# Optimization experiments

Hardware: AMD Instinct MI355X
Metric: run time of the kernel (lower is better)

The kernel has to match this reference:

```python
import jax, jax.numpy as jnp
import numpy as np

B, S, H, NH = 2, 2048, 4096, 32
D = H // NH  # head_dim = 128
ROPE_THETA = 10000.0


def setup_inputs() -> dict:
    key = jax.random.key(0)
    k0, k1, k2 = jax.random.split(key, 3)
    hidden_states = jax.random.normal(k0, (B, S, H), dtype=jnp.float32) * 0.02
    w_pack = jax.random.normal(k1, (H, 3 * H), dtype=jnp.float32) * 0.02  # fused QKV weight
    w_o = jax.random.normal(k2, (H, H), dtype=jnp.float32) * 0.02         # o_proj weight
    positions = jnp.broadcast_to(jnp.arange(S, dtype=jnp.int32), (B, S))
    return {"positions": positions, "hidden_states": hidden_states, "w_pack": w_pack, "w_o": w_o}


def _rope(x, positions):
    # neox-style rotary embedding (vLLM get_rope default), x: [B, S, NH, D]
    half = D // 2
    inv_freq = 1.0 / (ROPE_THETA ** (jnp.arange(0, half, dtype=jnp.float32) * 2.0 / D))
    freqs = positions.astype(jnp.float32)[..., None] * inv_freq  # [B, S, half]
    cos = jnp.cos(freqs)[:, :, None, :]  # [B, S, 1, half]
    sin = jnp.sin(freqs)[:, :, None, :]
    x1, x2 = x[..., :half], x[..., half:]
    return jnp.concatenate([x1 * cos - x2 * sin, x2 * cos + x1 * sin], axis=-1)


def reference(positions, hidden_states, w_pack, w_o):
    # fused QKV projection
    qkv = jnp.einsum('bsh,hf->bsf', hidden_states, w_pack)
    q, k, v = jnp.split(qkv, 3, axis=-1)
    q = q.reshape(B, S, NH, D)
    k = k.reshape(B, S, NH, D)
    v = v.reshape(B, S, NH, D)
    # RoPE on q, k
    q = _rope(q, positions)
    k = _rope(k, positions)
    # causal scaled dot-product attention
    scale = D ** -0.5
    scores = jnp.einsum('bqhd,bkhd->bhqk', q, k) * scale  # [B, NH, S, S]
    causal = jnp.tril(jnp.ones((S, S), dtype=bool))
    scores = jnp.where(causal[None, None], scores, jnp.finfo(scores.dtype).min)
    probs = jax.nn.softmax(scores, axis=-1)
    out = jnp.einsum('bhqk,bkhd->bqhd', probs, v).reshape(B, S, H)
    # output projection
    return jnp.einsum('bsh,hf->bsf', out, w_o)
```

## Files before the change

kernel.cpp:

```cpp
#include <hip/hip_runtime.h>

#define Sdim   2048
#define Hdim   4096
#define NHEADS 32
#define Dh     128
#define Mrows  4096
#define QKVLD  12288

typedef __attribute__((ext_vector_type(8))) short short8;
typedef __attribute__((ext_vector_type(4))) short short4v;
typedef __attribute__((ext_vector_type(4))) float f32x4;
typedef __attribute__((ext_vector_type(4))) float float4v;

__device__ __forceinline__ short f2bf(float f) {
  union { float f; unsigned u; } x; x.f = f;
  unsigned r = x.u + 0x7fffu + ((x.u >> 16) & 1u);
  return (short)(r >> 16);
}
__device__ __forceinline__ float bf2f(short s) {
  union { unsigned u; float f; } x; x.u = ((unsigned)(unsigned short)s) << 16;
  return x.f;
}

__device__ __forceinline__ void gload_lds16(const void* g, void* l) {
  __builtin_amdgcn_global_load_lds(
      (const __attribute__((address_space(1))) void*)g,
      (__attribute__((address_space(3))) void*)l, 16, 0, 0);
}

__global__ void k_prep(const float* __restrict__ hidden, short* __restrict__ Hbf,
                       const float* __restrict__ w_pack, short* __restrict__ Wpt) {
  __shared__ float t[64][65];
  const int tid = threadIdx.x;
  if (blockIdx.x < 8192) {
    int idx = blockIdx.x * 256 + tid;
    const float4v* s = (const float4v*)hidden + (size_t)idx * 2;
    float4v a = s[0], b = s[1];
    short8 o;
    o[0] = f2bf(a.x); o[1] = f2bf(a.y); o[2] = f2bf(a.z); o[3] = f2bf(a.w);
    o[4] = f2bf(b.x); o[5] = f2bf(b.y); o[6] = f2bf(b.z); o[7] = f2bf(b.w);
    *((short8*)Hbf + idx) = o;
  } else {
    const int idx = blockIdx.x - 8192;
    const int c0 = (idx % 192) * 64, r0 = (idx / 192) * 64;
    const int ir = tid >> 4, ic = (tid & 15) << 2;
#pragma unroll
    for (int p = 0; p < 4; ++p) {
      const float4v v = *(const float4v*)(w_pack + (size_t)(r0 + p * 16 + ir) * 12288 + c0 + ic);
      t[p * 16 + ir][ic] = v.x; t[p * 16 + ir][ic + 1] = v.y;
      t[p * 16 + ir][ic + 2] = v.z; t[p * 16 + ir][ic + 3] = v.w;
    }
    __syncthreads();
    const int oc = tid >> 3, orr = (tid & 7) << 3;
#pragma unroll
    for (int p = 0; p < 2; ++p) {
      int c = p * 32 + oc;
      short8 o;
#pragma unroll
      for (int j = 0; j < 8; ++j) o[j] = f2bf(t[orr + j][c]);
      *(short8*)(Wpt + (size_t)(c0 + c) * 4096 + r0 + orr) = o;
    }
  }
}

__device__ __forceinline__ void stage_half256(const short* G, int ld, int row0, int kcol,
                                              char* lds, int tid) {
#pragma unroll
  for (int j = 0; j < 2; ++j) {
    int p = j * 512 + tid;
    int r = p >> 3;
    int c = ((p & 7) ^ (r & 7)) << 3;
    gload_lds16(G + (size_t)(row0 + r) * ld + kcol + c,
                lds + ((j * 512 + (tid & 448)) << 4));
  }
}

#define MFMA_Q(qm, qn)                                                                   \
  do {                                                                                   \
    __builtin_amdgcn_s_setprio(1);                                                       \
    _Pragma("unroll")                                                                    \
    for (int m4 = 0; m4 < 4; ++m4)                                                       \
      _Pragma("unroll")                                                                  \
      for (int n2 = 0; n2 < 2; ++n2) {                                                   \
        acc[(qm)*4+m4][(qn)*2+n2] = __builtin_amdgcn_mfma_f32_16x16x32_bf16(             \
            av[m4][0], bv[(qn)*2+n2][0], acc[(qm)*4+m4][(qn)*2+n2], 0, 0, 0);            \
        acc[(qm)*4+m4][(qn)*2+n2] = __builtin_amdgcn_mfma_f32_16x16x32_bf16(             \
            av[m4][1], bv[(qn)*2+n2][1], acc[(qm)*4+m4][(qn)*2+n2], 0, 0, 0);            \
      }                                                                                  \
    __builtin_amdgcn_s_setprio(0);                                                       \
  } while (0)

#define PH_BARRIER()                    \
  do {                                  \
    __builtin_amdgcn_s_barrier();       \
    __builtin_amdgcn_sched_barrier(0);  \
  } while (0)

template<int MODE>
__global__ __launch_bounds__(512, 2) void k_gemm256(const short* __restrict__ A, int lda,
                                                    const short* __restrict__ Bt, int ldb,
                                                    void* __restrict__ Cp, int ldc,
                                                    int Ndim, int Kdim,
                                                    const int* __restrict__ positions,
                                                    short* __restrict__ Vtg) {
  __shared__ __align__(16) char smem[131072];
  const int tid  = threadIdx.x;
  const int lane = tid & 63;
  const int wave = tid >> 6;
  const int lo = lane & 15, hi = lane >> 4;
  const int wr = wave >> 2, wc = wave & 3;

  const int nblk = gridDim.x;
  const int lid = (blockIdx.x & 7) * (nblk >> 3) + (blockIdx.x >> 3);
  const int nbn = Ndim >> 8;
  const int bm0 = (lid / nbn) << 8;
  const int bn0 = (lid % nbn) << 8;

  f32x4 acc[8][4];
#pragma unroll
  for (int i = 0; i < 8; ++i)
#pragma unroll
    for (int j = 0; j < 4; ++j) acc[i][j] = (f32x4){0.f, 0.f, 0.f, 0.f};

  short8 av[4][2], bv[4][2];
  const int swz = (lo & 7) << 4;

  stage_half256(Bt, ldb, bn0,       0, smem + 32768,         tid);
  stage_half256(Bt, ldb, bn0 + 128, 0, smem + 32768 + 16384, tid);
  stage_half256(A,  lda, bm0,       0, smem,                 tid);
  stage_half256(A,  lda, bm0 + 128, 0, smem + 16384,         tid);

  const int NK = Kdim >> 6;
  for (int kt = 0; kt < NK; ++kt) {
    const int cur = kt & 1;
    const char* Ab = smem + cur * 65536 + wr * 16384;
    const char* Bb = smem + cur * 65536 + 32768;
    char* nA = smem + (cur ^ 1) * 65536;
    char* nB = nA + 32768;
    const int kc = (kt + 1) << 6;
    const bool pf = (kt + 1 < NK);

    if (pf) {
      stage_half256(Bt, ldb, bn0,       kc, nB,         tid);
      stage_half256(Bt, ldb, bn0 + 128, kc, nB + 16384, tid);
      asm volatile("s_waitcnt vmcnt(4)" ::: "memory");
    } else {
      asm volatile("s_waitcnt vmcnt(0)" ::: "memory");
    }
    PH_BARRIER();
#pragma unroll
    for (int m4 = 0; m4 < 4; ++m4)
#pragma unroll
      for (int ks = 0; ks < 2; ++ks)
        av[m4][ks] = *(const short8*)(Ab + (m4 * 16 + lo) * 128 + ((ks * 64 + hi * 16) ^ swz));
#pragma unroll
    for (int ni = 0; ni < 2; ++ni)
#pragma unroll
      for (int ks = 0; ks < 2; ++ks)
        bv[ni][ks] = *(const short8*)(Bb + (wc * 16 + ni * 64 + lo) * 128 + ((ks * 64 + hi * 16) ^ swz));
    MFMA_Q(0, 0);
#pragma unroll
    for (int ni = 2; ni < 4; ++ni)
#pragma unroll
      for (int ks = 0; ks < 2; ++ks)
        bv[ni][ks] = *(const short8*)(Bb + (wc * 16 + ni * 64 + lo) * 128 + ((ks * 64 + hi * 16) ^ swz));

    if (pf) {
      stage_half256(A, lda, bm0,       kc, nA,         tid);
      stage_half256(A, lda, bm0 + 128, kc, nA + 16384, tid);
    }
    PH_BARRIER();
    MFMA_Q(0, 1);
#pragma unroll
    for (int m4 = 0; m4 < 4; ++m4)
#pragma unroll
      for (int ks = 0; ks < 2; ++ks)
        av[m4][ks] = *(const short8*)(Ab + ((64 + m4 * 16 + lo) * 128) + ((ks * 64 + hi * 16) ^ swz));

    PH_BARRIER();
    MFMA_Q(1, 0);

    PH_BARRIER();
    MFMA_Q(1, 1);
  }

  if (MODE == 0) {
#pragma unroll
    for (int mi = 0; mi < 8; ++mi)
#pragma unroll
      for (int r = 0; r < 4; ++r) {
        int row = bm0 + wr * 128 + mi * 16 + hi * 4 + r;
#pragma unroll
        for (int ni = 0; ni < 4; ++ni) {
          int col = bn0 + wc * 16 + ni * 64 + lo;
          ((float*)Cp)[(size_t)row * ldc + col] = acc[mi][ni][r];
        }
      }
  } else if (bn0 < 8192) {
    short* qkvb = (short*)Cp;
    const int dd = wc * 16 + lo;
    const float inv = exp2f((float)dd * -0.2076205059304570f);
    const int row00 = bm0 + wr * 128 + hi * 4;
    float cm, sm, c1, s1, c16, s16;
    sincosf((float)positions[row00] * inv, &sm, &cm);
    sincosf(inv, &s1, &c1);
    sincosf(16.0f * inv, &s16, &c16);
#pragma unroll
    for (int mi = 0; mi < 8; ++mi) {
      float c = cm, s = sm;
#pragma unroll
      for (int r = 0; r < 4; ++r) {
        int row = row00 + mi * 16 + r;
        size_t base = (size_t)row * ldc + bn0 + wc * 16 + lo;
        float x1 = acc[mi][0][r], x2 = acc[mi][1][r];
        qkvb[base]       = f2bf(x1 * c - x2 * s);
        qkvb[base + 64]  = f2bf(x2 * c + x1 * s);
        float x3 = acc[mi][2][r], x4 = acc[mi][3][r];
        qkvb[base + 128] = f2bf(x3 * c - x4 * s);
        qkvb[base + 192] = f2bf(x4 * c + x3 * s);
        float cn = c * c1 - s * s1, sn = s * c1 + c * s1;
        c = cn; s = sn;
      }
      float cn = cm * c16 - sm * s16, sn = sm * c16 + cm * s16;
      cm = cn; sm = sn;
    }
  } else {
    const int b = bm0 >> 11;
    const int s0 = (bm0 & 2047) + wr * 128;
#pragma unroll
    for (int mi = 0; mi < 8; ++mi)
#pragma unroll
      for (int ni = 0; ni < 4; ++ni) {
        int col = bn0 - 8192 + wc * 16 + ni * 64 + lo;
        int h = col >> 7, d = col & 127;
        short4v o;
#pragma unroll
        for (int r = 0; r < 4; ++r) o[r] = f2bf(acc[mi][ni][r]);
        *(short4v*)(Vtg + (size_t)((b * 32 + h) * 128 + d) * Sdim + s0 + mi * 16 + hi * 4) = o;
      }
  }
}

__device__ __forceinline__ void stage_kv(const short* Kb, const short* Vtb, int kv0,
                                         char* kbuf, char* vbuf, int tid, int wave) {
#pragma unroll
  for (int i = 0; i < 4; ++i) {
    int p = i * 256 + tid;
    int r = p >> 4;
    int c = (p & 15) ^ (r & 7);
    gload_lds16(Kb + (size_t)(kv0 + r) * QKVLD + (c << 3),
                kbuf + ((i * 256 + wave * 64) << 4));
  }
#pragma unroll
  for (int i = 0; i < 4; ++i) {
    int p = i * 256 + tid;
    int r = p >> 3;
    int c = (p & 7) ^ (r & 7);
    gload_lds16(Vtb + (size_t)r * Sdim + kv0 + (c << 3),
                vbuf + ((i * 256 + wave * 64) << 4));
  }
}

__global__ __launch_bounds__(256, 2) void k_attn(short* __restrict__ qkv,
                                                 const short* __restrict__ Vt,
                                                 const float* __restrict__ w_o,
                                                 short* __restrict__ Wot) {
  __shared__ __align__(16) char smem[81920];
  const int tid  = threadIdx.x;

  if (blockIdx.x >= 1024) {
    float (*t)[65] = (float(*)[65])smem;
    const int idx = blockIdx.x - 1024;
    const int c0 = (idx & 63) << 6, r0 = (idx >> 6) << 6;
    const int ir = tid >> 4, ic = (tid & 15) << 2;
#pragma unroll
    for (int p = 0; p < 4; ++p) {
      const float4v v = *(const float4v*)(w_o + (size_t)(r0 + p * 16 + ir) * 4096 + c0 + ic);
      t[p * 16 + ir][ic] = v.x; t[p * 16 + ir][ic + 1] = v.y;
      t[p * 16 + ir][ic + 2] = v.z; t[p * 16 + ir][ic + 3] = v.w;
    }
    __syncthreads();
    const int oc = tid >> 3, orr = (tid & 7) << 3;
#pragma unroll
    for (int p = 0; p < 2; ++p) {
      int c = p * 32 + oc;
      short8 o;
#pragma unroll
      for (int j = 0; j < 8; ++j) o[j] = f2bf(t[orr + j][c]);
      *(short8*)(Wot + (size_t)(c0 + c) * 4096 + r0 + orr) = o;
    }
    return;
  }

  const int lane = tid & 63;
  const int wave = tid >> 6;
  const int lo = lane & 15, hi = lane >> 4;

  const int bid = blockIdx.x;
  const int lid = (bid & 7) * 128 + (bid >> 3);
  const int bh = lid >> 4;
  const int qt = 15 - (lid & 15);
  const int b = bh >> 5, h = bh & 31;
  const int q0 = qt << 7;

  short* base = qkv + (size_t)b * Sdim * QKVLD;
  const short* Qb = base + h * Dh;
  const short* Kb = base + Hdim + h * Dh;
  const short* Vtb = Vt + (size_t)(b * 32 + h) * 128 * Sdim;
  const int qrow0 = q0 + wave * 32;

  short* Pw = (short*)(smem + 65536 + wave * 4096);

  const float SEXP = 0.088388347648318447f * 1.4426950408889634f;

  short8 qf[2][4];
#pragma unroll
  for (int mi = 0; mi < 2; ++mi)
#pragma unroll
    for (int ks = 0; ks < 4; ++ks) {
      qf[mi][ks] = *(const short8*)(Qb + (size_t)(qrow0 + mi * 16 + lo) * QKVLD + ks * 32 + hi * 8);
#pragma unroll
      for (int j = 0; j < 8; ++j)
        qf[mi][ks][j] = f2bf(bf2f(qf[mi][ks][j]) * SEXP);
    }

  f32x4 acc_o[2][9];
  float m_run[2][4];
#pragma unroll
  for (int mi = 0; mi < 2; ++mi) {
#pragma unroll
    for (int nf = 0; nf < 9; ++nf) acc_o[mi][nf] = (f32x4){0.f, 0.f, 0.f, 0.f};
#pragma unroll
    for (int r = 0; r < 4; ++r) m_run[mi][r] = -1e30f;
  }

  short8 vones;
#pragma unroll
  for (int j = 0; j < 8; ++j) vones[j] = (short)0x3F80;

  const int nkv = (q0 + 128) >> 6;
  const int swz = (lo & 7) << 4;

  stage_kv(Kb, Vtb, 0, smem, smem + 16384, tid, wave);
  __syncthreads();

  int cur = 0;
  for (int kvt = 0; kvt < nkv; ++kvt) {
    const int kv0 = kvt << 6;
    if (kvt + 1 < nkv)
      stage_kv(Kb, Vtb, kv0 + 64, smem + (cur ^ 1) * 32768,
               smem + (cur ^ 1) * 32768 + 16384, tid, wave);

    if (kv0 <= qrow0 + 31) {
      const char* kl = smem + cur * 32768;
      const char* vl = smem + cur * 32768 + 16384;

      f32x4 accs[2][4];
#pragma unroll
      for (int mi = 0; mi < 2; ++mi)
#pragma unroll
        for (int nf = 0; nf < 4; ++nf) accs[mi][nf] = (f32x4){0.f, 0.f, 0.f, 0.f};
#pragma unroll
      for (int ks = 0; ks < 4; ++ks) {
        short8 kf[4];
#pragma unroll
        for (int nf = 0; nf < 4; ++nf) {
          int r = nf * 16 + lo;
          kf[nf] = *(const short8*)(kl + r * 256 + ((ks * 64 + hi * 16) ^ swz));
        }
        __builtin_amdgcn_s_setprio(1);
#pragma unroll
        for (int mi = 0; mi < 2; ++mi)
#pragma unroll
          for (int nf = 0; nf < 4; ++nf)
            accs[mi][nf] = __builtin_amdgcn_mfma_f32_16x16x32_bf16(qf[mi][ks], kf[nf], accs[mi][nf], 0, 0, 0);
        __builtin_amdgcn_s_setprio(0);
      }

      const bool needmask = (kv0 + 63 > qrow0);
      float pmax[2][4];
      bool okall = true;
#pragma unroll
      for (int mi = 0; mi < 2; ++mi) {
#pragma unroll
        for (int r = 0; r < 4; ++r) {
          const int qrow = qrow0 + mi * 16 + hi * 4 + r;
          if (needmask) {
#pragma unroll
            for (int nf = 0; nf < 4; ++nf) {
              int col = kv0 + nf * 16 + lo;
              accs[mi][nf][r] = (col <= qrow) ? accs[mi][nf][r] : -1e30f;
            }
          }
          float tmax = fmaxf(fmaxf(accs[mi][0][r], accs[mi][1][r]),
                             fmaxf(accs[mi][2][r], accs[mi][3][r]));
#pragma unroll
          for (int off = 1; off < 16; off <<= 1)
            tmax = fmaxf(tmax, __shfl_xor(tmax, off, 64));
          pmax[mi][r] = tmax;
          okall = okall && (tmax <= m_run[mi][r] + 8.0f);
        }
      }
      if (!__all(okall)) {
#pragma unroll
        for (int mi = 0; mi < 2; ++mi)
#pragma unroll
          for (int r = 0; r < 4; ++r) {
            float mnew = fmaxf(m_run[mi][r], pmax[mi][r]);
            float alpha = exp2f(m_run[mi][r] - mnew);
            m_run[mi][r] = mnew;
#pragma unroll
            for (int nf = 0; nf < 9; ++nf) acc_o[mi][nf][r] *= alpha;
          }
      }
#pragma unroll
      for (int mi = 0; mi < 2; ++mi)
#pragma unroll
        for (int r = 0; r < 4; ++r) {
          const int prow = mi * 16 + hi * 4 + r;
          const int psw = prow & 7;
#pragma unroll
          for (int nf = 0; nf < 4; ++nf) {
            float p = exp2f(accs[mi][nf][r] - m_run[mi][r]);
            int col = nf * 16 + lo;
            Pw[(prow << 6) + (((col >> 3) ^ psw) << 3) + (col & 7)] = f2bf(p);
          }
        }

#pragma unroll
      for (int ks = 0; ks < 2; ++ks) {
        short8 pf[2];
#pragma unroll
        for (int mi = 0; mi < 2; ++mi) {
          int prow = mi * 16 + lo;
          pf[mi] = *(const short8*)((const char*)Pw + prow * 128 + (((ks * 4 + hi) ^ (prow & 7)) << 4));
        }
        __builtin_amdgcn_s_setprio(1);
#pragma unroll
        for (int nf = 0; nf < 9; ++nf) {
          short8 vf;
          if (nf < 8) {
            int row = nf * 16 + lo;
            vf = *(const short8*)(vl + row * 128 + ((ks * 64 + hi * 16) ^ swz));
          } else {
            vf = vones;
          }
#pragma unroll
          for (int mi = 0; mi < 2; ++mi)
            acc_o[mi][nf] = __builtin_amdgcn_mfma_f32_16x16x32_bf16(pf[mi], vf, acc_o[mi][nf], 0, 0, 0);
        }
        __builtin_amdgcn_s_setprio(0);
      }
    }

    __syncthreads();
    cur ^= 1;
  }

  short* Osm = (short*)smem;
#pragma unroll
  for (int mi = 0; mi < 2; ++mi)
#pragma unroll
    for (int r = 0; r < 4; ++r) {
      float inv = 1.0f / acc_o[mi][8][r];
      int row = wave * 32 + mi * 16 + hi * 4 + r;
#pragma unroll
      for (int nf = 0; nf < 8; ++nf)
        Osm[row * 128 + nf * 16 + lo] = f2bf(acc_o[mi][nf][r] * inv);
    }
  __syncthreads();
  short* Ob = base + h * Dh;
#pragma unroll
  for (int it = 0; it < 8; ++it) {
    int chunk = it * 256 + tid;
    int row = chunk >> 4, c8 = chunk & 15;
    *(short8*)(Ob + (size_t)(q0 + row) * QKVLD + c8 * 8) =
        *(const short8*)(Osm + row * 128 + c8 * 8);
  }
}

extern "C" void kernel_launch(void* const* d_in, const int* in_sizes, int n_in,
                              void* d_out, int out_size, void* d_ws, size_t ws_size,
                              hipStream_t stream) {
  const int*   positions = (const int*)d_in[0];
  const float* hidden    = (const float*)d_in[1];
  const float* w_pack    = (const float*)d_in[2];
  const float* w_o       = (const float*)d_in[3];
  float* out = (float*)d_out;

  char* ws = (char*)d_ws;
  short* Wpt  = (short*)ws;
  short* qkvb = (short*)(ws + (size_t)12288 * 4096 * 2);
  short* Wot  = (short*)ws;
  short* Hbf  = (short*)d_out;
  short* Vtg  = (short*)((char*)d_out + ((size_t)32 << 20));

  k_prep<<<20480, 256, 0, stream>>>(hidden, Hbf, w_pack, Wpt);
  k_gemm256<1><<<dim3(768), 512, 0, stream>>>(Hbf, 4096, Wpt, 4096, qkvb, QKVLD, 12288, 4096,
                                              positions, Vtg);
  k_attn<<<dim3(5120), 256, 0, stream>>>(qkvb, Vtg, w_o, Wot);
  k_gemm256<0><<<dim3(256), 512, 0, stream>>>(qkvb, QKVLD, Wot, 4096, out, 4096, 4096, 4096,
                                              nullptr, nullptr);
}
```

Before: 718.0 us.

## Restructure GEMM main loop into 8-phase ping-pong with finer-grained quarter-tile prefetch

Replaces the two-stage double-buffered GEMM loop with an unrolled-by-two, eight-phase schedule. Global-to-LDS loads are issued as 64-row quarter tiles interleaved across the MFMA phases, with explicit vmcnt/lgkmcnt waits and barriers around each MFMA block. The aim is to spread memory traffic more evenly and overlap LDS reads with matrix math, in the style of HipBLASLt-like 256x256 schedules. This adds more barriers per iteration, relies on hand-tuned wait counts that must match the issued loads, and assumes the K tile count is even.

New measurement: 739.6 us. +3.0%, slower.

```diff
diff --git a/kernel.cpp b/kernel.cpp
--- a/kernel.cpp
+++ b/kernel.cpp
@@ -63,16 +63,11 @@
   }
 }
 
-__device__ __forceinline__ void stage_half256(const short* G, int ld, int row0, int kcol,
-                                              char* lds, int tid) {
-#pragma unroll
-  for (int j = 0; j < 2; ++j) {
-    int p = j * 512 + tid;
-    int r = p >> 3;
-    int c = ((p & 7) ^ (r & 7)) << 3;
-    gload_lds16(G + (size_t)(row0 + r) * ld + kcol + c,
-                lds + ((j * 512 + (tid & 448)) << 4));
-  }
+__device__ __forceinline__ void stage_q(const short* G, int ld, int row0, int kcol,
+                                        char* lds, int tid) {
+  int r = tid >> 3;
+  int c = ((tid & 7) ^ (r & 7)) << 3;
+  gload_lds16(G + (size_t)(row0 + r) * ld + kcol + c, lds + ((tid & 448) << 4));
 }
 
 #define MFMA_Q(qm, qn)                                                                   \
@@ -90,11 +85,31 @@
     __builtin_amdgcn_s_setprio(0);                                                       \
   } while (0)
 
-#define PH_BARRIER()                    \
-  do {                                  \
-    __builtin_amdgcn_s_barrier();       \
-    __builtin_amdgcn_sched_barrier(0);  \
-  } while (0)
+#define LDA(SBASE, QM)                                                                    \
+  _Pragma("unroll")                                                                       \
+  for (int m4 = 0; m4 < 4; ++m4)                                                          \
+    _Pragma("unroll")                                                                     \
+    for (int ks = 0; ks < 2; ++ks)                                                        \
+      av[m4][ks] = *(const short8*)((SBASE) + wr * 16384 +                                \
+                   (((QM) * 64 + m4 * 16 + lo) * 128) + ((ks * 64 + hi * 16) ^ swz));
+
+#define LDB(SBASE, NI0)                                                                   \
+  _Pragma("unroll")                                                                       \
+  for (int nn = 0; nn < 2; ++nn)                                                          \
+    _Pragma("unroll")                                                                     \
+    for (int ks = 0; ks < 2; ++ks)                                                        \
+      bv[(NI0)+nn][ks] = *(const short8*)((SBASE) +                                       \
+                   ((wc * 16 + ((NI0)+nn) * 64 + lo) * 128) + ((ks * 64 + hi * 16) ^ swz));
+
+#define PHASE_TAIL(QM, QN)                                \
+  __builtin_amdgcn_s_barrier();                           \
+  asm volatile("s_waitcnt lgkmcnt(0)" ::: "memory");      \
+  __builtin_amdgcn_sched_barrier(0);                      \
+  MFMA_Q(QM, QN);                                         \
+  __builtin_amdgcn_s_barrier();                           \
+  __builtin_amdgcn_sched_barrier(0);
+
+#define VM6() asm volatile("s_waitcnt vmcnt(6)" ::: "memory")
 
 template<int MODE>
 __global__ __launch_bounds__(512, 2) void k_gemm256(const short* __restrict__ A, int lda,
@@ -125,63 +140,89 @@
   short8 av[4][2], bv[4][2];
   const int swz = (lo & 7) << 4;
 
-  stage_half256(Bt, ldb, bn0,       0, smem + 32768,         tid);
-  stage_half256(Bt, ldb, bn0 + 128, 0, smem + 32768 + 16384, tid);
-  stage_half256(A,  lda, bm0,       0, smem,                 tid);
-  stage_half256(A,  lda, bm0 + 128, 0, smem + 16384,         tid);
+  char* S0A = smem;
+  char* S0B = smem + 32768;
+  char* S1A = smem + 65536;
+  char* S1B = smem + 98304;
+
+  stage_q(A,  lda, bm0,       0, S0A,         tid);
+  stage_q(A,  lda, bm0 + 64,  0, S0A + 8192,  tid);
+  stage_q(A,  lda, bm0 + 128, 0, S0A + 16384, tid);
+  stage_q(A,  lda, bm0 + 192, 0, S0A + 24576, tid);
+  stage_q(Bt, ldb, bn0,       0, S0B,         tid);
+  stage_q(Bt, ldb, bn0 + 64,  0, S0B + 8192,  tid);
+  stage_q(Bt, ldb, bn0 + 128, 0, S0B + 16384, tid);
+  stage_q(Bt, ldb, bn0 + 192, 0, S0B + 24576, tid);
+  stage_q(A,  lda, bm0,       64, S1A,         tid);
+  stage_q(A,  lda, bm0 + 128, 64, S1A + 16384, tid);
+  stage_q(Bt, ldb, bn0,       64, S1B,         tid);
+  stage_q(Bt, ldb, bn0 + 64,  64, S1B + 8192,  tid);
+  asm volatile("s_waitcnt vmcnt(0)" ::: "memory");
+  __builtin_amdgcn_s_barrier();
 
   const int NK = Kdim >> 6;
-  for (int kt = 0; kt < NK; ++kt) {
-    const int cur = kt & 1;
-    const char* Ab = smem + cur * 65536 + wr * 16384;
-    const char* Bb = smem + cur * 65536 + 32768;
-    char* nA = smem + (cur ^ 1) * 65536;
-    char* nB = nA + 32768;
-    const int kc = (kt + 1) << 6;
-    const bool pf = (kt + 1 < NK);
-
+  const int NIT = NK >> 1;
+  for (int it = 0; it < NIT; ++it) {
+    const int kc1 = ((it << 1) + 1) << 6;
+    const int kc2 = ((it << 1) + 2) << 6;
+    const int kc3 = ((it << 1) + 3) << 6;
+    const bool pf = ((it << 1) + 2 < NK);
+
+    LDA(S0A, 0); LDB(S0B, 0);
+    stage_q(Bt, ldb, bn0 + 128, kc1, S1B + 16384, tid);
+    stage_q(Bt, ldb, bn0 + 192, kc1, S1B + 24576, tid);
+    asm volatile("s_waitcnt lgkmcnt(8)" ::: "memory");
+    PHASE_TAIL(0, 0)
+
+    LDB(S0B, 2);
+    stage_q(A, lda, bm0 + 64,  kc1, S1A + 8192,  tid);
+    stage_q(A, lda, bm0 + 192, kc1, S1A + 24576, tid);
+    VM6();
+    PHASE_TAIL(0, 1)
+
+    LDA(S0A, 1);
     if (pf) {
-      stage_half256(Bt, ldb, bn0,       kc, nB,         tid);
-      stage_half256(Bt, ldb, bn0 + 128, kc, nB + 16384, tid);
-      asm volatile("s_waitcnt vmcnt(4)" ::: "memory");
-    } else {
-      asm volatile("s_waitcnt vmcnt(0)" ::: "memory");
-    }
-    PH_BARRIER();
-#pragma unroll
-    for (int m4 = 0; m4 < 4; ++m4)
-#pragma unroll
-      for (int ks = 0; ks < 2; ++ks)
-        av[m4][ks] = *(const short8*)(Ab + (m4 * 16 + lo) * 128 + ((ks * 64 + hi * 16) ^ swz));
-#pragma unroll
-    for (int ni = 0; ni < 2; ++ni)
-#pragma unroll
-      for (int ks = 0; ks < 2; ++ks)
-        bv[ni][ks] = *(const short8*)(Bb + (wc * 16 + ni * 64 + lo) * 128 + ((ks * 64 + hi * 16) ^ swz));
-    MFMA_Q(0, 0);
-#pragma unroll
-    for (int ni = 2; ni < 4; ++ni)
-#pragma unroll
-      for (int ks = 0; ks < 2; ++ks)
-        bv[ni][ks] = *(const short8*)(Bb + (wc * 16 + ni * 64 + lo) * 128 + ((ks * 64 + hi * 16) ^ swz));
+      stage_q(A, lda, bm0,       kc2, S0A,         tid);
+      stage_q(A, lda, bm0 + 128, kc2, S0A + 16384, tid);
+    }
+    PHASE_TAIL(1, 0)
 
     if (pf) {
-      stage_half256(A, lda, bm0,       kc, nA,         tid);
-      stage_half256(A, lda, bm0 + 128, kc, nA + 16384, tid);
-    }
-    PH_BARRIER();
-    MFMA_Q(0, 1);
-#pragma unroll
-    for (int m4 = 0; m4 < 4; ++m4)
-#pragma unroll
-      for (int ks = 0; ks < 2; ++ks)
-        av[m4][ks] = *(const short8*)(Ab + ((64 + m4 * 16 + lo) * 128) + ((ks * 64 + hi * 16) ^ swz));
-
-    PH_BARRIER();
-    MFMA_Q(1, 0);
-
-    PH_BARRIER();
-    MFMA_Q(1, 1);
+      stage_q(Bt, ldb, bn0,      kc2, S0B,        tid);
+      stage_q(Bt, ldb, bn0 + 64, kc2, S0B + 8192, tid);
+    }
+    VM6();
+    PHASE_TAIL(1, 1)
+
+    LDA(S1A, 0); LDB(S1B, 0);
+    if (pf) {
+      stage_q(Bt, ldb, bn0 + 128, kc2, S0B + 16384, tid);
+      stage_q(Bt, ldb, bn0 + 192, kc2, S0B + 24576, tid);
+    }
+    asm volatile("s_waitcnt lgkmcnt(8)" ::: "memory");
+    PHASE_TAIL(0, 0)
+
+    LDB(S1B, 2);
+    if (pf) {
+      stage_q(A, lda, bm0 + 64,  kc2, S0A + 8192,  tid);
+      stage_q(A, lda, bm0 + 192, kc2, S0A + 24576, tid);
+    }
+    VM6();
+    PHASE_TAIL(0, 1)
+
+    LDA(S1A, 1);
+    if (pf) {
+      stage_q(A, lda, bm0,       kc3, S1A,         tid);
+      stage_q(A, lda, bm0 + 128, kc3, S1A + 16384, tid);
+    }
+    PHASE_TAIL(1, 0)
+
+    if (pf) {
+      stage_q(Bt, ldb, bn0,      kc3, S1B,        tid);
+      stage_q(Bt, ldb, bn0 + 64, kc3, S1B + 8192, tid);
+    }
+    VM6();
+    PHASE_TAIL(1, 1)
   }
 
   if (MODE == 0) {
```
